# Kernel optimization log

Hardware: AMD Instinct MI355X
Metric: run time of the kernel (lower is better)

Reference implementation:

```python
import jax, jax.numpy as jnp
import numpy as np

SCORE_THRESH = 0.25
NMS_THRESH = 0.45
DETECTIONS = 100   # self.detections
K_CAND = 300       # fixed pre-NMS candidate count (jit-friendly stand-in for torch.where filtering)
STRIDES = (8, 16, 32)


def setup_inputs() -> dict:
    key = jax.random.key(0)
    ks = jax.random.split(key, 5)
    pred_p3 = jax.random.normal(ks[0], (16, 80, 80, 3, 85), jnp.float32)
    pred_p4 = jax.random.normal(ks[1], (16, 40, 40, 3, 85), jnp.float32)
    pred_p5 = jax.random.normal(ks[2], (16, 20, 20, 3, 85), jnp.float32)
    anchors = jnp.array([[[10, 13], [16, 30], [33, 23]],
                         [[30, 61], [62, 45], [59, 119]],
                         [[116, 90], [156, 198], [373, 326]]], jnp.float32)
    image_shapes = jnp.full((16, 2), 640, jnp.int32)  # (h, w) per image
    scale_factors = jax.random.uniform(ks[3], (16,), jnp.float32, 0.5, 1.5)
    return {"pred_p3": pred_p3, "pred_p4": pred_p4, "pred_p5": pred_p5,
            "anchors": anchors, "image_shapes": image_shapes,
            "scale_factors": scale_factors, "max_size": 4096}


def _decode_level(p, stride, anchor_wh):
    # p: [B,H,W,A,5+C] already sigmoided
    B, H, W, A, _ = p.shape
    gx = jnp.arange(W, dtype=p.dtype)
    gy = jnp.arange(H, dtype=p.dtype)
    grid = jnp.stack(jnp.meshgrid(gx, gy, indexing='xy'), axis=-1)  # [H,W,2] = (x,y)
    xy = (2.0 * p[..., :2] - 0.5 + grid[None, :, :, None, :]) * stride
    wh = 4.0 * p[..., 2:4] ** 2 * anchor_wh  # anchor_wh: [A,2]
    box = jnp.concatenate([xy, wh], axis=-1).reshape(B, H * W * A, 4)
    obj = p[..., 4].reshape(B, H * W * A)
    cls = p[..., 5:].reshape(B, H * W * A, -1)
    return box, obj, cls


def _pairwise_iou(b):  # b: [K,4] xyxy
    area = (b[:, 2] - b[:, 0]) * (b[:, 3] - b[:, 1])
    lt = jnp.maximum(b[:, None, :2], b[None, :, :2])
    rb = jnp.minimum(b[:, None, 2:], b[None, :, 2:])
    wh = jnp.clip(rb - lt, 0.0)
    inter = wh[..., 0] * wh[..., 1]
    return inter / (area[:, None] + area[None, :] - inter + 1e-9)


def _nms_image(boxes, scores, labels, im_shape, scale, max_size):
    # boxes [K,4], scores [K] sorted desc, labels [K] int
    w = im_shape[1].astype(boxes.dtype)
    h = im_shape[0].astype(boxes.dtype)
    boxes = jnp.stack([jnp.clip(boxes[:, 0], 0.0, w), jnp.clip(boxes[:, 1], 0.0, h),
                       jnp.clip(boxes[:, 2], 0.0, w), jnp.clip(boxes[:, 3], 0.0, h)], axis=1)
    # class-offset boxes (batched_nms)
    bn = jax.lax.stop_gradient(boxes + (labels.astype(boxes.dtype) * max_size)[:, None])
    iou = _pairwise_iou(bn)
    s_ng = jax.lax.stop_gradient(scores)
    K = boxes.shape[0]
    ar = jnp.arange(K)

    def body(i, keep):
        active = keep[i] & (s_ng[i] > SCORE_THRESH)
        return keep & ~((iou[i] > NMS_THRESH) & (ar > i) & active)

    keep = jax.lax.fori_loop(0, K, body, jnp.ones(K, bool))
    final = jnp.where(keep & (s_ng > SCORE_THRESH), scores, 0.0)
    det_s, det_i = jax.lax.top_k(final, DETECTIONS)
    det_b = boxes[det_i] / scale
    det_l = labels[det_i].astype(boxes.dtype)
    return jnp.concatenate([det_b, det_s[:, None], det_l[:, None]], axis=1)  # [D,6]


def reference(pred_p3, pred_p4, pred_p5, anchors, image_shapes, scale_factors, max_size):
    boxes_l, obj_l, cls_l = [], [], []
    for i, (pred, stride) in enumerate(zip((pred_p3, pred_p4, pred_p5), STRIDES)):
        p = jax.nn.sigmoid(pred)
        b, o, c = _decode_level(p, float(stride), anchors[i])
        boxes_l.append(b); obj_l.append(o); cls_l.append(c)
    boxes = jnp.concatenate(boxes_l, axis=1)   # [B,N,4] cxcywh
    obj = jnp.concatenate(obj_l, axis=1)       # [B,N]
    cls = jnp.concatenate(cls_l, axis=1)       # [B,N,C]
    # cxcywh -> xyxy
    cx, cy, ww, hh = boxes[..., 0], boxes[..., 1], boxes[..., 2], boxes[..., 3]
    boxes = jnp.stack([cx - ww / 2, cy - hh / 2, cx + ww / 2, cy + hh / 2], axis=-1)
    B, N, C = cls.shape
    logits = obj[..., None] * cls              # [B,N,C]
    valid = (obj[..., None] > SCORE_THRESH) & (logits > SCORE_THRESH)
    flat = jnp.where(valid, logits, 0.0).reshape(B, N * C)
    vals, idx = jax.lax.top_k(flat, K_CAND)    # sorted desc per image
    aidx = idx // C
    labels = idx % C
    cand_boxes = jnp.take_along_axis(boxes, aidx[..., None], axis=1)  # [B,K,4]
    out = jax.vmap(_nms_image, in_axes=(0, 0, 0, 0, 0, None))(
        cand_boxes, vals, labels, image_shapes, scale_factors, jnp.float32(max_size))
    return out  # [B, DETECTIONS, 6] = (x1,y1,x2,y2,score,label)
```

## Files before the change

kernel.cpp:

```cpp
#include <hip/hip_runtime.h>
#include <cstdint>
#include <cstddef>

#define BATCH 16
#define NCLS 80
#define NANCH 25200
#define G 48
#define NCHUNK 525
#define TOTCH (BATCH * NCHUNK)
#define CPB 4
#define ABINS 512
#define SBINS 1024
#define ACAP 2048
#define SCAP 2048
#define TILE 64
#define KC 300
#define DET 100
#define SCORE_T 0.25f
#define NMS_T 0.45f

__device__ __forceinline__ float sg(float x) { return 1.0f / (1.0f + expf(-x)); }

__device__ __forceinline__ const float* anchor_base(const float* p3, const float* p4,
                                                    const float* p5, int b, int n) {
    if (n < 19200) return p3 + ((size_t)b * 19200 + n) * 85;
    if (n < 24000) return p4 + ((size_t)b * 4800 + (n - 19200)) * 85;
    return p5 + ((size_t)b * 1200 + (n - 24000)) * 85;
}

struct Chunk { const float4* p; int outbase; };
__device__ __forceinline__ Chunk chunk_of(int g, const float* p3, const float* p4,
                                          const float* p5) {
    Chunk ck;
    int b = g / NCHUNK, ch = g % NCHUNK;
    const float* src; int a0, lvlN, gbase;
    if (ch < 400)      { src = p3; a0 = ch * G;         lvlN = 19200; gbase = 0; }
    else if (ch < 500) { src = p4; a0 = (ch - 400) * G; lvlN = 4800;  gbase = 19200; }
    else               { src = p5; a0 = (ch - 500) * G; lvlN = 1200;  gbase = 24000; }
    ck.p = (const float4*)(src + ((size_t)b * lvlN + a0) * 85);
    ck.outbase = b * NANCH + gbase + a0;
    return ck;
}

__global__ __launch_bounds__(256) void k_max(const float* __restrict__ p3,
                                             const float* __restrict__ p4,
                                             const float* __restrict__ p5,
                                             float* __restrict__ gmax) {
    __shared__ __align__(16) float buf[G * 85];
    __shared__ float pmax[5 * G];
    int tid = threadIdx.x;
    int g0 = blockIdx.x * CPB;
    Chunk cur = chunk_of(g0, p3, p4, p5);
    float4 pre[4];
#pragma unroll
    for (int r = 0; r < 4; r++) {
        int i = tid + r * 256;
        pre[r] = (i < (G * 85 / 4)) ? cur.p[i] : make_float4(0.f, 0.f, 0.f, 0.f);
    }
    for (int it = 0; it < CPB; ++it) {
#pragma unroll
        for (int r = 0; r < 4; r++) {
            int i = tid + r * 256;
            if (i < (G * 85 / 4)) ((float4*)buf)[i] = pre[r];
        }
        Chunk nxt = cur;
        if (it + 1 < CPB) {
            nxt = chunk_of(g0 + it + 1, p3, p4, p5);
#pragma unroll
            for (int r = 0; r < 4; r++) {
                int i = tid + r * 256;
                pre[r] = (i < (G * 85 / 4)) ? nxt.p[i] : make_float4(0.f, 0.f, 0.f, 0.f);
            }
        }
        __syncthreads();
        if (tid < 240) {
            int a = tid % G, part = tid / G;
            const float* base = buf + a * 85 + 5 + part * 16;
            float m = base[0];
#pragma unroll
            for (int k = 1; k < 16; k++) m = fmaxf(m, base[k]);
            pmax[part * G + a] = m;
        }
        __syncthreads();
        if (tid < G) {
            float m = pmax[tid];
#pragma unroll
            for (int p = 1; p < 5; p++) m = fmaxf(m, pmax[p * G + tid]);
            float obj = sg(buf[tid * 85 + 4]);
            float v = 0.0f;
            if (obj > SCORE_T) v = obj * sg(m);
            gmax[cur.outbase + tid] = v;
        }
        __syncthreads();
        cur = nxt;
    }
}

union Ovl {
    struct { float tile[TILE * 85]; } p1;
    struct {
        unsigned long long msk[KC * 5];
        float4 bx[KC];
        int lab[KC];
        float sc2[KC];
        float ar[KC];
        unsigned long long keep[5];
        unsigned int actw[10];
        int wpref[6];
        int order[DET];
        int okept[DET];
    } p2;
};

__global__ __launch_bounds__(1024) void k_img(
    const float* __restrict__ p3, const float* __restrict__ p4, const float* __restrict__ p5,
    const float* __restrict__ anchors, const int* __restrict__ imshapes,
    const float* __restrict__ scalef, const float* __restrict__ gmax,
    float* __restrict__ out) {
    __shared__ unsigned int hist[SBINS];
    __shared__ int alist[ACAP];
    __shared__ __align__(16) Ovl u;
    __shared__ float cs[SCAP];
    __shared__ unsigned int ci[SCAP];
    __shared__ float sv[KC];
    __shared__ unsigned int si[KC];
    __shared__ unsigned int acnt, scnt;
    __shared__ int TaS, TsS;

    int b = blockIdx.x;
    int tid = threadIdx.x;
    const float* gm = gmax + (size_t)b * NANCH;

    hist[tid & (SBINS - 1)] = 0u;
    if (tid == 0) { acnt = 0u; scnt = 0u; TaS = 0; TsS = 0; }
    __syncthreads();
    for (int n = tid; n < NANCH; n += 1024) {
        float v = gm[n];
        if (v > SCORE_T) {
            int bin = (int)((v - SCORE_T) * (ABINS / 0.75f));
            bin = bin < 0 ? 0 : (bin > ABINS - 1 ? ABINS - 1 : bin);
            atomicAdd(&hist[bin], 1u);
        }
    }
    __syncthreads();
    unsigned int run = 0;
    if (tid < ABINS) run = hist[tid];
    __syncthreads();
    for (int off = 1; off < ABINS; off <<= 1) {
        unsigned int add = (tid < ABINS && tid + off < ABINS) ? hist[tid + off] : 0u;
        __syncthreads();
        if (tid < ABINS) { run += add; hist[tid] = run; }
        __syncthreads();
    }
    if (tid < ABINS && run >= KC && (tid == ABINS - 1 || hist[tid + 1] < KC)) TaS = tid;
    __syncthreads();
    int Ta = TaS;

    for (int n = tid; n < NANCH; n += 1024) {
        float v = gm[n];
        if (v > SCORE_T) {
            int bin = (int)((v - SCORE_T) * (ABINS / 0.75f));
            bin = bin < 0 ? 0 : (bin > ABINS - 1 ? ABINS - 1 : bin);
            if (bin >= Ta) {
                unsigned int pos = atomicAdd(&acnt, 1u);
                if (pos < ACAP) alist[pos] = n;
            }
        }
    }
    __syncthreads();
    int M = (int)(acnt < ACAP ? acnt : ACAP);

    hist[tid] = 0u;
    __syncthreads();
    for (int t0 = 0; t0 < M; t0 += TILE) {
        int tc = min(TILE, M - t0);
        for (int idx = tid; idx < tc * 85; idx += 1024) {
            int a = idx / 85, f = idx - a * 85;
            u.p1.tile[idx] = anchor_base(p3, p4, p5, b, alist[t0 + a])[f];
        }
        __syncthreads();
        for (int idx = tid; idx < tc * 80; idx += 1024) {
            int a = idx / 80, c = idx - a * 80;
            float s = sg(u.p1.tile[a * 85 + 4]) * sg(u.p1.tile[a * 85 + 5 + c]);
            if (s > SCORE_T) {
                int bin = (int)((s - SCORE_T) * (SBINS / 0.75f));
                bin = bin < 0 ? 0 : (bin > SBINS - 1 ? SBINS - 1 : bin);
                atomicAdd(&hist[bin], 1u);
            }
        }
        __syncthreads();
    }
    run = hist[tid];
    __syncthreads();
    for (int off = 1; off < SBINS; off <<= 1) {
        unsigned int add = (tid + off < SBINS) ? hist[tid + off] : 0u;
        __syncthreads();
        run += add;
        hist[tid] = run;
        __syncthreads();
    }
    if (run >= KC && (tid == SBINS - 1 || hist[tid + 1] < KC)) TsS = tid;
    __syncthreads();
    int Ts = TsS;

    for (int t0 = 0; t0 < M; t0 += TILE) {
        int tc = min(TILE, M - t0);
        for (int idx = tid; idx < tc * 85; idx += 1024) {
            int a = idx / 85, f = idx - a * 85;
            u.p1.tile[idx] = anchor_base(p3, p4, p5, b, alist[t0 + a])[f];
        }
        __syncthreads();
        for (int idx = tid; idx < tc * 80; idx += 1024) {
            int a = idx / 80, c = idx - a * 80;
            float s = sg(u.p1.tile[a * 85 + 4]) * sg(u.p1.tile[a * 85 + 5 + c]);
            if (s > SCORE_T) {
                int bin = (int)((s - SCORE_T) * (SBINS / 0.75f));
                bin = bin < 0 ? 0 : (bin > SBINS - 1 ? SBINS - 1 : bin);
                if (bin >= Ts) {
                    unsigned int pos = atomicAdd(&scnt, 1u);
                    if (pos < SCAP) {
                        cs[pos] = s;
                        ci[pos] = (unsigned int)(alist[t0 + a] * NCLS + c);
                    }
                }
            }
        }
        __syncthreads();
    }
    int nc = (int)(scnt < SCAP ? scnt : SCAP);

    if (tid < KC) { sv[tid] = 0.f; si[tid] = 0xffffffffu; }
    __syncthreads();
    for (int i = tid; i < nc; i += 1024) {
        float s = cs[i];
        unsigned int ii = ci[i];
        int r = 0;
        for (int j = 0; j < nc; j++) {
            float sj = cs[j];
            unsigned int ij = ci[j];
            if (sj > s || (sj == s && ij < ii)) r++;
        }
        if (r < KC) { sv[r] = s; si[r] = ii; }
    }
    __syncthreads();
    int valid = nc < KC ? nc : KC;

    if (tid < KC) {
        int i = tid;
        if (i < valid) {
            unsigned int fi = si[i];
            int n = (int)(fi / NCLS), c = (int)(fi % NCLS);
            int lvl = (n < 19200) ? 0 : (n < 24000 ? 1 : 2);
            const int offl[3] = {0, 19200, 24000};
            const int Wl[3] = {80, 40, 20};
            const int cntl[3] = {19200, 4800, 1200};
            const float strl[3] = {8.f, 16.f, 32.f};
            const float* pp = lvl == 0 ? p3 : (lvl == 1 ? p4 : p5);
            int nl = n - offl[lvl];
            int a = nl % 3, cell = nl / 3;
            int gx = cell % Wl[lvl], gy = cell / Wl[lvl];
            const float* pb = pp + ((size_t)b * cntl[lvl] + nl) * 85;
            float s0 = sg(pb[0]), s1 = sg(pb[1]), s2 = sg(pb[2]), s3 = sg(pb[3]);
            float stride = strl[lvl];
            float aw = anchors[(lvl * 3 + a) * 2 + 0];
            float ah = anchors[(lvl * 3 + a) * 2 + 1];
            float cx = (2.0f * s0 - 0.5f + (float)gx) * stride;
            float cy = (2.0f * s1 - 0.5f + (float)gy) * stride;
            float bw = 4.0f * s2 * s2 * aw;
            float bh = 4.0f * s3 * s3 * ah;
            float hf = (float)imshapes[b * 2 + 0];
            float wf = (float)imshapes[b * 2 + 1];
            float x1 = cx - bw / 2.0f, y1 = cy - bh / 2.0f;
            float x2 = cx + bw / 2.0f, y2 = cy + bh / 2.0f;
            x1 = fminf(fmaxf(x1, 0.f), wf);
            y1 = fminf(fmaxf(y1, 0.f), hf);
            x2 = fminf(fmaxf(x2, 0.f), wf);
            y2 = fminf(fmaxf(y2, 0.f), hf);
            u.p2.bx[i] = make_float4(x1, y1, x2, y2);
            u.p2.lab[i] = c;
            u.p2.sc2[i] = sv[i];
            u.p2.ar[i] = (x2 - x1) * (y2 - y1);
        } else {
            u.p2.bx[i] = make_float4(0, 0, 0, 0);
            u.p2.lab[i] = -1 - i;
            u.p2.sc2[i] = 0.f;
            u.p2.ar[i] = 0.f;
        }
    }
    __syncthreads();

    if (tid < 10) u.p2.actw[tid] = 0u;
    for (int t = tid; t < KC * 5; t += 1024) {
        int i = t / 5, w = t % 5;
        float4 bi = u.p2.bx[i];
        int li = u.p2.lab[i];
        float ai = u.p2.ar[i];
        unsigned long long m = 0ull;
        for (int tb = 0; tb < 64; tb++) {
            int j = w * 64 + tb;
            if (j < KC && j > i && u.p2.lab[j] == li) {
                float4 bj = u.p2.bx[j];
                float ltx = fmaxf(bi.x, bj.x), lty = fmaxf(bi.y, bj.y);
                float rbx = fminf(bi.z, bj.z), rby = fminf(bi.w, bj.w);
                float iw = fmaxf(rbx - ltx, 0.f), ih = fmaxf(rby - lty, 0.f);
                float inter = iw * ih;
                float iou = inter / (ai + u.p2.ar[j] - inter + 1e-9f);
                if (iou > NMS_T) m |= (1ull << tb);
            }
        }
        u.p2.msk[t] = m;
    }
    __syncthreads();

    for (int i = tid; i < KC; i += 1024) {
        unsigned long long nz = u.p2.msk[i * 5] | u.p2.msk[i * 5 + 1] | u.p2.msk[i * 5 + 2] |
                                u.p2.msk[i * 5 + 3] | u.p2.msk[i * 5 + 4];
        if (nz) atomicOr(&u.p2.actw[i >> 5], 1u << (i & 31));
    }
    __syncthreads();
    if (tid == 0) {
        u.p2.keep[0] = u.p2.keep[1] = u.p2.keep[2] = u.p2.keep[3] = u.p2.keep[4] = ~0ull;
        for (int w = 0; w < 10; w++) {
            unsigned int mw = u.p2.actw[w];
            while (mw) {
                int bpos = __ffs(mw) - 1;
                mw &= mw - 1;
                int i = w * 32 + bpos;
                if ((u.p2.keep[i >> 6] >> (i & 63)) & 1ull) {
#pragma unroll
                    for (int r = 0; r < 5; r++) u.p2.keep[r] &= ~u.p2.msk[i * 5 + r];
                }
            }
        }
        int s = 0;
        for (int w = 0; w < 5; w++) {
            unsigned long long kw = u.p2.keep[w];
            if (w == 4) kw &= (1ull << 44) - 1ull;
            u.p2.wpref[w] = s;
            s += (int)__popcll(kw);
        }
        u.p2.wpref[5] = s;
    }
    __syncthreads();

    if (tid < KC) {
        int w = tid >> 6, bp = tid & 63;
        unsigned long long kw = u.p2.keep[w];
        bool kept = (kw >> bp) & 1ull;
        int r = u.p2.wpref[w] + (int)__popcll(kw & ((1ull << bp) - 1ull));
        if (kept) {
            if (r < DET) { u.p2.order[r] = tid; u.p2.okept[r] = 1; }
        } else {
            int nr = u.p2.wpref[5] + (tid - r);
            if (nr < DET) { u.p2.order[nr] = tid; u.p2.okept[nr] = 0; }
        }
    }
    __syncthreads();

    if (tid < DET) {
        int o = u.p2.order[tid];
        float scale = scalef[b];
        float4 bb = u.p2.bx[o];
        float s = (u.p2.okept[tid] && o < valid) ? u.p2.sc2[o] : 0.f;
        float lb = (o < valid) ? (float)u.p2.lab[o] : 0.f;
        float* po = out + ((size_t)b * DET + tid) * 6;
        po[0] = bb.x / scale;
        po[1] = bb.y / scale;
        po[2] = bb.z / scale;
        po[3] = bb.w / scale;
        po[4] = s;
        po[5] = lb;
    }
}

extern "C" void kernel_launch(void* const* d_in, const int* in_sizes, int n_in,
                              void* d_out, int out_size, void* d_ws, size_t ws_size,
                              hipStream_t stream) {
    const float* p3 = (const float*)d_in[0];
    const float* p4 = (const float*)d_in[1];
    const float* p5 = (const float*)d_in[2];
    const float* anchors = (const float*)d_in[3];
    const int* imshapes = (const int*)d_in[4];
    const float* scalef = (const float*)d_in[5];
    float* out = (float*)d_out;

    float* gmax = (float*)d_ws;

    k_max<<<TOTCH / CPB, 256, 0, stream>>>(p3, p4, p5, gmax);
    k_img<<<BATCH, 1024, 0, stream>>>(p3, p4, p5, anchors, imshapes, scalef, gmax, out);
}
```

Measured before the change: 271.6 us.

## Fuse into one cooperative kernel and spread per-image candidate selection across blocks

Replaces the two-kernel pipeline with a single cooperative kernel of 256 blocks that uses grid-wide syncs between phases. The per-image anchor filter and both score-histogram passes, previously done by only 16 blocks, are now split across 16 blocks per image, with global atomics merging histograms and candidate lists. Only the final sort and NMS stay at one block per image. This aims to remove the serial bottleneck of 16 large blocks on a GPU with many more CUs, at the cost of four grid barriers and global atomics. The old two-kernel path remains as a fallback if the cooperative launch fails.

```diff
diff --git a/kernel.cpp b/kernel.cpp
--- a/kernel.cpp
+++ b/kernel.cpp
@@ -1,6 +1,9 @@
 #include <hip/hip_runtime.h>
+#include <hip/hip_cooperative_groups.h>
 #include <cstdint>
 #include <cstddef>
+
+namespace cg = cooperative_groups;
 
 #define BATCH 16
 #define NCLS 80
@@ -8,16 +11,20 @@
 #define G 48
 #define NCHUNK 525
 #define TOTCH (BATCH * NCHUNK)
+#define NBLK 256
+#define NTHR 1024
 #define CPB 4
 #define ABINS 512
 #define SBINS 1024
-#define ACAP 2048
-#define SCAP 2048
+#define CAP 2048
 #define TILE 64
 #define KC 300
 #define DET 100
 #define SCORE_T 0.25f
 #define NMS_T 0.45f
+#define SLICE (NANCH / 16)
+
+typedef unsigned long long ull;
 
 __device__ __forceinline__ float sg(float x) { return 1.0f / (1.0f + expf(-x)); }
 
@@ -42,6 +49,339 @@
     return ck;
 }
 
+__global__ __launch_bounds__(1024) void k_all(
+    const float* __restrict__ p3, const float* __restrict__ p4, const float* __restrict__ p5,
+    const float* __restrict__ anchors, const int* __restrict__ imshapes,
+    const float* __restrict__ scalef,
+    float* __restrict__ gmax, unsigned int* __restrict__ shist,
+    unsigned int* __restrict__ acnt, unsigned int* __restrict__ scnt,
+    int* __restrict__ alist, uint2* __restrict__ cand, float* __restrict__ out) {
+    __shared__ __align__(16) unsigned char smem[40960];
+    __shared__ int TaS, TsS;
+    cg::grid_group grid = cg::this_grid();
+    int tid = threadIdx.x;
+
+    {
+        int gid = blockIdx.x * NTHR + tid;
+        int zn = BATCH * SBINS + 2 * BATCH;
+        for (int i = gid; i < zn; i += NBLK * NTHR) shist[i] = 0u;
+
+        float* buf = (float*)smem;
+        float* pmax = (float*)(smem + 16320);
+        Chunk cur = chunk_of(blockIdx.x, p3, p4, p5);
+        float4 pre = (tid < 1020) ? cur.p[tid] : make_float4(0.f, 0.f, 0.f, 0.f);
+        for (int k = 0; k < 33; k++) {
+            int g = blockIdx.x + NBLK * k;
+            if (g >= TOTCH) break;
+            if (tid < 1020) ((float4*)buf)[tid] = pre;
+            int gn = g + NBLK;
+            Chunk nxt = cur;
+            if (gn < TOTCH) {
+                nxt = chunk_of(gn, p3, p4, p5);
+                if (tid < 1020) pre = nxt.p[tid];
+            }
+            __syncthreads();
+            if (tid < 240) {
+                int a = tid % G, part = tid / G;
+                const float* base = buf + a * 85 + 5 + part * 16;
+                float m = base[0];
+#pragma unroll
+                for (int q = 1; q < 16; q++) m = fmaxf(m, base[q]);
+                pmax[part * G + a] = m;
+            }
+            __syncthreads();
+            if (tid < G) {
+                float m = pmax[tid];
+#pragma unroll
+                for (int p = 1; p < 5; p++) m = fmaxf(m, pmax[p * G + tid]);
+                float obj = sg(buf[tid * 85 + 4]);
+                float v = 0.0f;
+                if (obj > SCORE_T) v = obj * sg(m);
+                gmax[cur.outbase + tid] = v;
+            }
+            __syncthreads();
+            cur = nxt;
+        }
+    }
+    __threadfence();
+    grid.sync();
+
+    {
+        int b = blockIdx.x >> 4, sub = blockIdx.x & 15;
+        unsigned int* hist = (unsigned int*)smem;
+        if (tid < ABINS) hist[tid] = 0u;
+        if (tid == 0) TaS = 0;
+        __syncthreads();
+        const float* gm = gmax + (size_t)b * NANCH;
+        for (int n = tid; n < NANCH; n += NTHR) {
+            float v = gm[n];
+            if (v > SCORE_T) {
+                int bin = (int)((v - SCORE_T) * (ABINS / 0.75f));
+                bin = bin < 0 ? 0 : (bin > ABINS - 1 ? ABINS - 1 : bin);
+                atomicAdd(&hist[bin], 1u);
+            }
+        }
+        __syncthreads();
+        unsigned int run = (tid < ABINS) ? hist[tid] : 0u;
+        __syncthreads();
+        for (int off = 1; off < ABINS; off <<= 1) {
+            unsigned int add = (tid < ABINS && tid + off < ABINS) ? hist[tid + off] : 0u;
+            __syncthreads();
+            if (tid < ABINS) { run += add; hist[tid] = run; }
+            __syncthreads();
+        }
+        if (tid < ABINS && run >= KC && (tid == ABINS - 1 || hist[tid + 1] < KC)) TaS = tid;
+        __syncthreads();
+        int Ta = TaS;
+        for (int n = sub * SLICE + tid; n < (sub + 1) * SLICE; n += NTHR) {
+            float v = gm[n];
+            if (v > SCORE_T) {
+                int bin = (int)((v - SCORE_T) * (ABINS / 0.75f));
+                bin = bin < 0 ? 0 : (bin > ABINS - 1 ? ABINS - 1 : bin);
+                if (bin >= Ta) {
+                    unsigned int pos = atomicAdd(&acnt[b], 1u);
+                    if (pos < CAP) alist[b * CAP + pos] = n;
+                }
+            }
+        }
+    }
+    __threadfence();
+    grid.sync();
+
+    {
+        int b = blockIdx.x >> 4, sub = blockIdx.x & 15;
+        unsigned int* hist = (unsigned int*)smem;
+        hist[tid] = 0u;
+        __syncthreads();
+        int M = (int)acnt[b]; if (M > CAP) M = CAP;
+        int Mb = (M > sub) ? (M - sub + 15) / 16 : 0;
+        for (int w = tid; w < Mb * NCLS; w += NTHR) {
+            int t = w / NCLS, c = w - t * NCLS;
+            int n = alist[b * CAP + sub + 16 * t];
+            const float* base = anchor_base(p3, p4, p5, b, n);
+            float s = sg(base[4]) * sg(base[5 + c]);
+            if (s > SCORE_T) {
+                int bin = (int)((s - SCORE_T) * (SBINS / 0.75f));
+                bin = bin < 0 ? 0 : (bin > SBINS - 1 ? SBINS - 1 : bin);
+                atomicAdd(&hist[bin], 1u);
+            }
+        }
+        __syncthreads();
+        if (hist[tid]) atomicAdd(&shist[b * SBINS + tid], hist[tid]);
+    }
+    __threadfence();
+    grid.sync();
+
+    {
+        int b = blockIdx.x >> 4, sub = blockIdx.x & 15;
+        unsigned int* hist = (unsigned int*)smem;
+        unsigned int run = shist[b * SBINS + tid];
+        if (tid == 0) TsS = 0;
+        hist[tid] = run;
+        __syncthreads();
+        for (int off = 1; off < SBINS; off <<= 1) {
+            unsigned int add = (tid + off < SBINS) ? hist[tid + off] : 0u;
+            __syncthreads();
+            run += add;
+            hist[tid] = run;
+            __syncthreads();
+        }
+        if (run >= KC && (tid == SBINS - 1 || hist[tid + 1] < KC)) TsS = tid;
+        __syncthreads();
+        int Ts = TsS;
+        int M = (int)acnt[b]; if (M > CAP) M = CAP;
+        int Mb = (M > sub) ? (M - sub + 15) / 16 : 0;
+        for (int w = tid; w < Mb * NCLS; w += NTHR) {
+            int t = w / NCLS, c = w - t * NCLS;
+            int n = alist[b * CAP + sub + 16 * t];
+            const float* base = anchor_base(p3, p4, p5, b, n);
+            float s = sg(base[4]) * sg(base[5 + c]);
+            if (s > SCORE_T) {
+                int bin = (int)((s - SCORE_T) * (SBINS / 0.75f));
+                bin = bin < 0 ? 0 : (bin > SBINS - 1 ? SBINS - 1 : bin);
+                if (bin >= Ts) {
+                    unsigned int pos = atomicAdd(&scnt[b], 1u);
+                    if (pos < CAP)
+                        cand[(size_t)b * CAP + pos] =
+                            make_uint2(__float_as_uint(s), (unsigned int)(n * NCLS + c));
+                }
+            }
+        }
+    }
+    __threadfence();
+    grid.sync();
+
+    if (blockIdx.x >= BATCH) return;
+    {
+        int b = blockIdx.x;
+        float*        cs    = (float*)smem;
+        unsigned int* ci    = (unsigned int*)(smem + 8192);
+        ull*          msk   = (ull*)(smem + 16384);
+        float4*       bx    = (float4*)(smem + 28384);
+        int*          lab   = (int*)(smem + 33184);
+        float*        sc2   = (float*)(smem + 34384);
+        float*        ar    = (float*)(smem + 35584);
+        float*        sv    = (float*)(smem + 36784);
+        unsigned int* si    = (unsigned int*)(smem + 37984);
+        ull*          keep  = (ull*)(smem + 39184);
+        unsigned int* actw  = (unsigned int*)(smem + 39224);
+        int*          wpref = (int*)(smem + 39264);
+        int*          order = (int*)(smem + 39288);
+        int*          okept = (int*)(smem + 39688);
+
+        int nc = (int)scnt[b];
+        if (nc > CAP) nc = CAP;
+        for (int i = tid; i < nc; i += NTHR) {
+            uint2 cc = cand[(size_t)b * CAP + i];
+            cs[i] = __uint_as_float(cc.x);
+            ci[i] = cc.y;
+        }
+        if (tid < KC) { sv[tid] = 0.f; si[tid] = 0xffffffffu; }
+        if (tid < 10) actw[tid] = 0u;
+        __syncthreads();
+
+        for (int i = tid; i < nc; i += NTHR) {
+            float s = cs[i];
+            unsigned int ii = ci[i];
+            int r = 0;
+            for (int j = 0; j < nc; j++) {
+                float sj = cs[j];
+                unsigned int ij = ci[j];
+                if (sj > s || (sj == s && ij < ii)) r++;
+            }
+            if (r < KC) { sv[r] = s; si[r] = ii; }
+        }
+        __syncthreads();
+        int valid = nc < KC ? nc : KC;
+
+        if (tid < KC) {
+            int i = tid;
+            if (i < valid) {
+                unsigned int fi = si[i];
+                int n = (int)(fi / NCLS), c = (int)(fi % NCLS);
+                int lvl = (n < 19200) ? 0 : (n < 24000 ? 1 : 2);
+                const int offl[3] = {0, 19200, 24000};
+                const int Wl[3] = {80, 40, 20};
+                const int cntl[3] = {19200, 4800, 1200};
+                const float strl[3] = {8.f, 16.f, 32.f};
+                const float* pp = lvl == 0 ? p3 : (lvl == 1 ? p4 : p5);
+                int nl = n - offl[lvl];
+                int a = nl % 3, cell = nl / 3;
+                int gx = cell % Wl[lvl], gy = cell / Wl[lvl];
+                const float* pb = pp + ((size_t)b * cntl[lvl] + nl) * 85;
+                float s0 = sg(pb[0]), s1 = sg(pb[1]), s2 = sg(pb[2]), s3 = sg(pb[3]);
+                float stride = strl[lvl];
+                float aw = anchors[(lvl * 3 + a) * 2 + 0];
+                float ah = anchors[(lvl * 3 + a) * 2 + 1];
+                float cx = (2.0f * s0 - 0.5f + (float)gx) * stride;
+                float cy = (2.0f * s1 - 0.5f + (float)gy) * stride;
+                float bw = 4.0f * s2 * s2 * aw;
+                float bh = 4.0f * s3 * s3 * ah;
+                float hf = (float)imshapes[b * 2 + 0];
+                float wf = (float)imshapes[b * 2 + 1];
+                float x1 = cx - bw / 2.0f, y1 = cy - bh / 2.0f;
+                float x2 = cx + bw / 2.0f, y2 = cy + bh / 2.0f;
+                x1 = fminf(fmaxf(x1, 0.f), wf);
+                y1 = fminf(fmaxf(y1, 0.f), hf);
+                x2 = fminf(fmaxf(x2, 0.f), wf);
+                y2 = fminf(fmaxf(y2, 0.f), hf);
+                bx[i] = make_float4(x1, y1, x2, y2);
+                lab[i] = c;
+                sc2[i] = sv[i];
+                ar[i] = (x2 - x1) * (y2 - y1);
+            } else {
+                bx[i] = make_float4(0, 0, 0, 0);
+                lab[i] = -1 - i;
+                sc2[i] = 0.f;
+                ar[i] = 0.f;
+            }
+        }
+        __syncthreads();
+
+        for (int t = tid; t < KC * 5; t += NTHR) {
+            int i = t / 5, w = t % 5;
+            float4 bi = bx[i];
+            int li = lab[i];
+            float ai = ar[i];
+            ull m = 0ull;
+            for (int tb = 0; tb < 64; tb++) {
+                int j = w * 64 + tb;
+                if (j < KC && j > i && lab[j] == li) {
+                    float4 bj = bx[j];
+                    float ltx = fmaxf(bi.x, bj.x), lty = fmaxf(bi.y, bj.y);
+                    float rbx = fminf(bi.z, bj.z), rby = fminf(bi.w, bj.w);
+                    float iw = fmaxf(rbx - ltx, 0.f), ih = fmaxf(rby - lty, 0.f);
+                    float inter = iw * ih;
+                    float iou = inter / (ai + ar[j] - inter + 1e-9f);
+                    if (iou > NMS_T) m |= (1ull << tb);
+                }
+            }
+            msk[t] = m;
+        }
+        __syncthreads();
+
+        for (int i = tid; i < KC; i += NTHR) {
+            ull nz = msk[i * 5] | msk[i * 5 + 1] | msk[i * 5 + 2] |
+                     msk[i * 5 + 3] | msk[i * 5 + 4];
+            if (nz) atomicOr(&actw[i >> 5], 1u << (i & 31));
+        }
+        __syncthreads();
+        if (tid == 0) {
+            keep[0] = keep[1] = keep[2] = keep[3] = keep[4] = ~0ull;
+            for (int w = 0; w < 10; w++) {
+                unsigned int mw = actw[w];
+                while (mw) {
+                    int bpos = __ffs(mw) - 1;
+                    mw &= mw - 1;
+                    int i = w * 32 + bpos;
+                    if ((keep[i >> 6] >> (i & 63)) & 1ull) {
+#pragma unroll
+                        for (int r = 0; r < 5; r++) keep[r] &= ~msk[i * 5 + r];
+                    }
+                }
+            }
+            int s = 0;
+            for (int w = 0; w < 5; w++) {
+                ull kw = keep[w];
+                if (w == 4) kw &= (1ull << 44) - 1ull;
+                wpref[w] = s;
+                s += (int)__popcll(kw);
+            }
+            wpref[5] = s;
+        }
+        __syncthreads();
+
+        if (tid < KC) {
+            int w = tid >> 6, bp = tid & 63;
+            ull kw = keep[w];
+            bool kept = (kw >> bp) & 1ull;
+            int r = wpref[w] + (int)__popcll(kw & ((1ull << bp) - 1ull));
+            if (kept) {
+                if (r < DET) { order[r] = tid; okept[r] = 1; }
+            } else {
+                int nr = wpref[5] + (tid - r);
+                if (nr < DET) { order[nr] = tid; okept[nr] = 0; }
+            }
+        }
+        __syncthreads();
+
+        if (tid < DET) {
+            int o = order[tid];
+            float scale = scalef[b];
+            float4 bb = bx[o];
+            float s = (okept[tid] && o < valid) ? sc2[o] : 0.f;
+            float lb = (o < valid) ? (float)lab[o] : 0.f;
+            float* po = out + ((size_t)b * DET + tid) * 6;
+            po[0] = bb.x / scale;
+            po[1] = bb.y / scale;
+            po[2] = bb.z / scale;
+            po[3] = bb.w / scale;
+            po[4] = s;
+            po[5] = lb;
+        }
+    }
+}
+
 __global__ __launch_bounds__(256) void k_max(const float* __restrict__ p3,
                                              const float* __restrict__ p4,
                                              const float* __restrict__ p5,
@@ -99,12 +439,12 @@
 union Ovl {
     struct { float tile[TILE * 85]; } p1;
     struct {
-        unsigned long long msk[KC * 5];
+        ull msk[KC * 5];
         float4 bx[KC];
         int lab[KC];
         float sc2[KC];
         float ar[KC];
-        unsigned long long keep[5];
+        ull keep[5];
         unsigned int actw[10];
         int wpref[6];
         int order[DET];
@@ -118,10 +458,10 @@
     const float* __restrict__ scalef, const float* __restrict__ gmax,
     float* __restrict__ out) {
     __shared__ unsigned int hist[SBINS];
-    __shared__ int alist[ACAP];
+    __shared__ int alist[CAP];
     __shared__ __align__(16) Ovl u;
-    __shared__ float cs[SCAP];
-    __shared__ unsigned int ci[SCAP];
+    __shared__ float cs[CAP];
+    __shared__ unsigned int ci[CAP];
     __shared__ float sv[KC];
     __shared__ unsigned int si[KC];
     __shared__ unsigned int acnt, scnt;
@@ -163,12 +503,12 @@
             bin = bin < 0 ? 0 : (bin > ABINS - 1 ? ABINS - 1 : bin);
             if (bin >= Ta) {
                 unsigned int pos = atomicAdd(&acnt, 1u);
-                if (pos < ACAP) alist[pos] = n;
-            }
-        }
-    }
-    __syncthreads();
-    int M = (int)(acnt < ACAP ? acnt : ACAP);
+                if (pos < CAP) alist[pos] = n;
+            }
+        }
+    }
+    __syncthreads();
+    int M = (int)(acnt < CAP ? acnt : CAP);
 
     hist[tid] = 0u;
     __syncthreads();
@@ -218,7 +558,7 @@
                 bin = bin < 0 ? 0 : (bin > SBINS - 1 ? SBINS - 1 : bin);
                 if (bin >= Ts) {
                     unsigned int pos = atomicAdd(&scnt, 1u);
-                    if (pos < SCAP) {
+                    if (pos < CAP) {
                         cs[pos] = s;
                         ci[pos] = (unsigned int)(alist[t0 + a] * NCLS + c);
                     }
@@ -227,7 +567,7 @@
         }
         __syncthreads();
     }
-    int nc = (int)(scnt < SCAP ? scnt : SCAP);
+    int nc = (int)(scnt < CAP ? scnt : CAP);
 
     if (tid < KC) { sv[tid] = 0.f; si[tid] = 0xffffffffu; }
     __syncthreads();
@@ -295,7 +635,7 @@
         float4 bi = u.p2.bx[i];
         int li = u.p2.lab[i];
         float ai = u.p2.ar[i];
-        unsigned long long m = 0ull;
+        ull m = 0ull;
         for (int tb = 0; tb < 64; tb++) {
             int j = w * 64 + tb;
             if (j < KC && j > i && u.p2.lab[j] == li) {
@@ -313,8 +653,8 @@
     __syncthreads();
 
     for (int i = tid; i < KC; i += 1024) {
-        unsigned long long nz = u.p2.msk[i * 5] | u.p2.msk[i * 5 + 1] | u.p2.msk[i * 5 + 2] |
-                                u.p2.msk[i * 5 + 3] | u.p2.msk[i * 5 + 4];
+        ull nz = u.p2.msk[i * 5] | u.p2.msk[i * 5 + 1] | u.p2.msk[i * 5 + 2] |
+                 u.p2.msk[i * 5 + 3] | u.p2.msk[i * 5 + 4];
         if (nz) atomicOr(&u.p2.actw[i >> 5], 1u << (i & 31));
     }
     __syncthreads();
@@ -334,7 +674,7 @@
         }
         int s = 0;
         for (int w = 0; w < 5; w++) {
-            unsigned long long kw = u.p2.keep[w];
+            ull kw = u.p2.keep[w];
             if (w == 4) kw &= (1ull << 44) - 1ull;
             u.p2.wpref[w] = s;
             s += (int)__popcll(kw);
@@ -345,7 +685,7 @@
 
     if (tid < KC) {
         int w = tid >> 6, bp = tid & 63;
-        unsigned long long kw = u.p2.keep[w];
+        ull kw = u.p2.keep[w];
         bool kept = (kw >> bp) & 1ull;
         int r = u.p2.wpref[w] + (int)__popcll(kw & ((1ull << bp) - 1ull));
         if (kept) {
@@ -385,7 +725,19 @@
     float* out = (float*)d_out;
 
     float* gmax = (float*)d_ws;
-
-    k_max<<<TOTCH / CPB, 256, 0, stream>>>(p3, p4, p5, gmax);
-    k_img<<<BATCH, 1024, 0, stream>>>(p3, p4, p5, anchors, imshapes, scalef, gmax, out);
+    uint2* cand = (uint2*)(gmax + BATCH * NANCH);
+    unsigned int* shist = (unsigned int*)(cand + BATCH * CAP);
+    unsigned int* acnt = shist + BATCH * SBINS;
+    unsigned int* scnt = acnt + BATCH;
+    int* alist = (int*)(scnt + BATCH);
+
+    void* args[] = {(void*)&p3, (void*)&p4, (void*)&p5, (void*)&anchors,
+                    (void*)&imshapes, (void*)&scalef, (void*)&gmax, (void*)&shist,
+                    (void*)&acnt, (void*)&scnt, (void*)&alist, (void*)&cand, (void*)&out};
+    hipError_t err = hipLaunchCooperativeKernel((const void*)k_all, dim3(NBLK), dim3(NTHR),
+                                                args, 0, stream);
+    if (err != hipSuccess) {
+        k_max<<<TOTCH / CPB, 256, 0, stream>>>(p3, p4, p5, gmax);
+        k_img<<<BATCH, 1024, 0, stream>>>(p3, p4, p5, anchors, imshapes, scalef, gmax, out);
+    }
 }
```

Result: slower. 681.2 us (+150.8%).
